# Kernel tuning notes

Hardware: AMD Instinct MI355X
Metric: run time of the kernel (lower is better)

The kernel has to match this reference:

```python
import jax, jax.numpy as jnp
import numpy as np

B, S, D, H, DFF = 2, 2048, 1024, 16, 4096
DK = D // H
EPS = 1e-6

def setup_inputs() -> dict:
    key = jax.random.key(0)
    ks = jax.random.split(key, 12)
    sc = 0.02
    inp = {
        "x": jax.random.normal(ks[0], (B, S, D), jnp.float32),
        "src_mask": jax.random.randint(ks[1], (B, 1, 1, S), 0, 2, jnp.int32),
        "wq": jax.random.normal(ks[2], (D, D), jnp.float32) * sc,
        "bq": jnp.zeros((D,), jnp.float32),
        "wk": jax.random.normal(ks[3], (D, D), jnp.float32) * sc,
        "bk": jnp.zeros((D,), jnp.float32),
        "wv": jax.random.normal(ks[4], (D, D), jnp.float32) * sc,
        "bv": jnp.zeros((D,), jnp.float32),
        "wo": jax.random.normal(ks[5], (D, D), jnp.float32) * sc,
        "bo": jnp.zeros((D,), jnp.float32),
        "w1": jax.random.normal(ks[6], (DFF, D), jnp.float32) * sc,
        "b1": jnp.zeros((DFF,), jnp.float32),
        "w2": jax.random.normal(ks[7], (D, DFF), jnp.float32) * sc,
        "b2": jnp.zeros((D,), jnp.float32),
        "a1": jnp.ones((1,), jnp.float32),
        "be1": jnp.zeros((1,), jnp.float32),
        "a2": jnp.ones((1,), jnp.float32),
        "be2": jnp.zeros((1,), jnp.float32),
    }
    return inp

def layer_norm(x, alpha, beta):
    # custom LN: unbiased std (ddof=1), scalar alpha/beta, divide by (std + eps)
    mean = jnp.mean(x, axis=-1, keepdims=True)
    std = jnp.std(x, axis=-1, keepdims=True, ddof=1)
    return alpha * (x - mean) / (std + EPS) + beta

def mha(x, mask, wq, bq, wk, bk, wv, bv, wo, bo):
    q = (x @ wq.T + bq).reshape(B, S, H, DK).transpose(0, 2, 1, 3)  # [B,H,S,DK]
    k = (x @ wk.T + bk).reshape(B, S, H, DK).transpose(0, 2, 1, 3)
    v = (x @ wv.T + bv).reshape(B, S, H, DK).transpose(0, 2, 1, 3)
    scores = jnp.einsum('bhqd,bhkd->bhqk', q, k) / jnp.sqrt(jnp.float32(DK))
    scores = jnp.where(mask == 0, jnp.float32(-1e9), scores)
    attn = jax.nn.softmax(scores, axis=-1)
    out = jnp.einsum('bhqk,bhkd->bhqd', attn, v)
    out = out.transpose(0, 2, 1, 3).reshape(B, S, D)
    return out @ wo.T + bo

def ffn(x, w1, b1, w2, b2):
    h = jax.nn.relu(x @ w1.T + b1)
    return h @ w2.T + b2

def reference(x, src_mask, wq, bq, wk, bk, wv, bv, wo, bo, w1, b1, w2, b2, a1, be1, a2, be2):
    # pre-norm residual 1: self-attention
    x = x + mha(layer_norm(x, a1, be1), src_mask, wq, bq, wk, bk, wv, bv, wo, bo)
    # pre-norm residual 2: FFN
    x = x + ffn(layer_norm(x, a2, be2), w1, b1, w2, b2)
    return x
```

## Files before the change

kernel.cpp:

```cpp
#include <hip/hip_runtime.h>

#define B_    2
#define S_    2048
#define D_    1024
#define H_    16
#define DK_   64
#define DFF_  4096
#define MROWS (B_*S_)

typedef float f32x4 __attribute__((ext_vector_type(4)));
typedef __bf16 bf16x8 __attribute__((ext_vector_type(8)));

static __device__ __forceinline__ unsigned short f2bf(float f) {
    union { float f; unsigned u; } a; a.f = f;
    unsigned u = a.u;
    u += 0x7FFF + ((u >> 16) & 1);
    return (unsigned short)(u >> 16);
}

static __device__ __forceinline__ void gload16(const unsigned short* g, unsigned short* l) {
    __builtin_amdgcn_global_load_lds((const __attribute__((address_space(1))) void*)g,
                                     (__attribute__((address_space(3))) void*)l, 16, 0, 0);
}

__global__ void cast_kernel(const float* __restrict__ in, unsigned short* __restrict__ out) {
    int i = blockIdx.x * blockDim.x + threadIdx.x;
    float4 v = ((const float4*)in)[i];
    ushort4 o;
    o.x = f2bf(v.x); o.y = f2bf(v.y); o.z = f2bf(v.z); o.w = f2bf(v.w);
    ((ushort4*)out)[i] = o;
}

__global__ __launch_bounds__(256) void ln_kernel(const float* __restrict__ x,
                                                 const float* __restrict__ alphap,
                                                 const float* __restrict__ betap,
                                                 unsigned short* __restrict__ out) {
    int row = blockIdx.x;
    int t = threadIdx.x;
    const float* xr = x + (size_t)row * D_;
    float4 v = ((const float4*)xr)[t];
    float s  = v.x + v.y + v.z + v.w;
    float s2 = v.x*v.x + v.y*v.y + v.z*v.z + v.w*v.w;
    #pragma unroll
    for (int o = 1; o < 64; o <<= 1) { s += __shfl_xor(s, o); s2 += __shfl_xor(s2, o); }
    __shared__ float ss[4], ss2[4];
    if ((t & 63) == 0) { ss[t >> 6] = s; ss2[t >> 6] = s2; }
    __syncthreads();
    float S  = ss[0] + ss[1] + ss[2] + ss[3];
    float S2 = ss2[0] + ss2[1] + ss2[2] + ss2[3];
    float mean = S * (1.f / (float)D_);
    float var  = (S2 - S * mean) / (float)(D_ - 1);
    float alpha = alphap[0], beta = betap[0];
    float inv = alpha / (sqrtf(fmaxf(var, 0.f)) + 1e-6f);
    ushort4 o4;
    o4.x = f2bf((v.x - mean) * inv + beta);
    o4.y = f2bf((v.y - mean) * inv + beta);
    o4.z = f2bf((v.z - mean) * inv + beta);
    o4.w = f2bf((v.w - mean) * inv + beta);
    ((ushort4*)(out + (size_t)row * D_))[t] = o4;
}

template<int BN, int EPI, int BIAS_ROW>
__global__ __launch_bounds__(256) void gemm_bt(const unsigned short* __restrict__ A,
                                               const unsigned short* __restrict__ W,
                                               const float* __restrict__ bias,
                                               const float* __restrict__ resid,
                                               unsigned short* __restrict__ outb,
                                               float* __restrict__ outf,
                                               int M, int N, int K) {
    constexpr int NI = BN / 32;
    __shared__ __align__(16) unsigned short As[128 * 64];
    __shared__ __align__(16) unsigned short Bs[BN * 64];
    const int t = threadIdx.x, lane = t & 63, w = t >> 6;
    const int m0 = blockIdx.y * 128, n0 = blockIdx.x * BN;
    const int wm = (w & 1) * 64;
    const int wn = (BN == 128) ? (w >> 1) * 64 : (w >> 1) * 32;
    const int l15 = lane & 15, l4 = lane >> 4;
    const int ar0 = w * 8 + (lane >> 3);
    const int ac0 = (lane & 7) * 8;

    f32x4 acc[4][NI];
    f32x4 z4 = {0.f, 0.f, 0.f, 0.f};
    #pragma unroll
    for (int i = 0; i < 4; i++)
        #pragma unroll
        for (int j = 0; j < NI; j++) acc[i][j] = z4;

    const unsigned short* Ap = A + (size_t)m0 * K;
    const unsigned short* Wp = W + (size_t)n0 * K;

    for (int k0 = 0; k0 < K; k0 += 64) {
        #pragma unroll
        for (int j = 0; j < 4; j++)
            gload16(Ap + (size_t)(j*32 + ar0) * K + k0 + ac0, &As[(j*4 + w) * 512]);
        #pragma unroll
        for (int j = 0; j < BN/32; j++)
            gload16(Wp + (size_t)(j*32 + ar0) * K + k0 + ac0, &Bs[(j*4 + w) * 512]);
        __syncthreads();

        #pragma unroll
        for (int ks = 0; ks < 2; ks++) {
            bf16x8 af[4], bfr[NI];
            #pragma unroll
            for (int mi = 0; mi < 4; mi++)
                af[mi] = *(const bf16x8*)&As[(wm + mi*16 + l15)*64 + ks*32 + l4*8];
            #pragma unroll
            for (int ni = 0; ni < NI; ni++)
                bfr[ni] = *(const bf16x8*)&Bs[(wn + ni*16 + l15)*64 + ks*32 + l4*8];
            #pragma unroll
            for (int mi = 0; mi < 4; mi++)
                #pragma unroll
                for (int ni = 0; ni < NI; ni++)
                    acc[mi][ni] = __builtin_amdgcn_mfma_f32_16x16x32_bf16(af[mi], bfr[ni], acc[mi][ni], 0, 0, 0);
        }
        __syncthreads();
    }

    #pragma unroll
    for (int mi = 0; mi < 4; mi++) {
        #pragma unroll
        for (int ni = 0; ni < NI; ni++) {
            int gc = n0 + wn + ni*16 + l15;
            float bc = BIAS_ROW ? 0.f : bias[gc];
            #pragma unroll
            for (int j = 0; j < 4; j++) {
                int gr = m0 + wm + mi*16 + 4*l4 + j;
                float val = acc[mi][ni][j] + (BIAS_ROW ? bias[gr] : bc);
                if (EPI == 1) val = fmaxf(val, 0.f);
                if (EPI == 2) {
                    val += resid[(size_t)gr * N + gc];
                    outf[(size_t)gr * N + gc] = val;
                } else {
                    outb[(size_t)gr * N + gc] = f2bf(val);
                }
            }
        }
    }
}

__global__ __launch_bounds__(256) void attn_kernel(const unsigned short* __restrict__ q,
                                                   const unsigned short* __restrict__ k,
                                                   const unsigned short* __restrict__ vt,
                                                   const int* __restrict__ mask,
                                                   unsigned short* __restrict__ out) {
    __shared__ __align__(16) unsigned short Ks[64][72], Vs[64][72], Ps[64][72];
    __shared__ int mS[64];
    const int t = threadIdx.x, lane = t & 63, w = t >> 6;
    const int l15 = lane & 15, l4 = lane >> 4;
    const int bh = blockIdx.y, b = bh >> 4, h = bh & 15;
    const int q0 = blockIdx.x * 64;
    const size_t headoff = ((size_t)b * S_) * D_ + (size_t)h * DK_;
    const unsigned short* qb = q + headoff + (size_t)q0 * D_;
    const unsigned short* kb = k + headoff;
    const unsigned short* vtb = vt + (size_t)(h * DK_) * MROWS + (size_t)b * S_;

    bf16x8 aq[2];
    #pragma unroll
    for (int ks = 0; ks < 2; ks++)
        aq[ks] = *(const bf16x8*)(qb + (size_t)(w*16 + l15) * D_ + ks*32 + l4*8);

    float m_[4], l_[4];
    f32x4 accd[4];
    f32x4 z4 = {0.f, 0.f, 0.f, 0.f};
    #pragma unroll
    for (int j = 0; j < 4; j++) { m_[j] = -INFINITY; l_[j] = 0.f; }
    #pragma unroll
    for (int dt = 0; dt < 4; dt++) accd[dt] = z4;

    const int r_ = t >> 3, c8_ = (t & 7) * 8;

    for (int kv0 = 0; kv0 < S_; kv0 += 64) {
        #pragma unroll
        for (int p = 0; p < 2; p++) {
            int r = r_ + p * 32;
            *(uint4*)&Ks[r][c8_] = *(const uint4*)(kb  + (size_t)(kv0 + r) * D_ + c8_);
            *(uint4*)&Vs[r][c8_] = *(const uint4*)(vtb + (size_t)r * MROWS + kv0 + c8_);
        }
        if (t < 64) mS[t] = mask[(size_t)b * S_ + kv0 + t];
        __syncthreads();

        f32x4 sc[4];
        #pragma unroll
        for (int nt = 0; nt < 4; nt++) sc[nt] = z4;
        #pragma unroll
        for (int nt = 0; nt < 4; nt++)
            #pragma unroll
            for (int ks = 0; ks < 2; ks++) {
                bf16x8 bk8 = *(const bf16x8*)&Ks[nt*16 + l15][ks*32 + 8*l4];
                sc[nt] = __builtin_amdgcn_mfma_f32_16x16x32_bf16(aq[ks], bk8, sc[nt], 0, 0, 0);
            }

        float sv[4][4];
        int mk[4];
        #pragma unroll
        for (int nt = 0; nt < 4; nt++) mk[nt] = mS[nt*16 + l15];
        #pragma unroll
        for (int nt = 0; nt < 4; nt++)
            #pragma unroll
            for (int j = 0; j < 4; j++)
                sv[nt][j] = (mk[nt] == 0) ? -1e9f : sc[nt][j] * 0.125f;

        float esc[4], rs[4];
        #pragma unroll
        for (int j = 0; j < 4; j++) {
            float mxx = fmaxf(fmaxf(sv[0][j], sv[1][j]), fmaxf(sv[2][j], sv[3][j]));
            #pragma unroll
            for (int o = 1; o < 16; o <<= 1) mxx = fmaxf(mxx, __shfl_xor(mxx, o));
            float mn = fmaxf(m_[j], mxx);
            esc[j] = __expf(m_[j] - mn);
            m_[j] = mn;
            rs[j] = 0.f;
        }
        float p[4][4];
        #pragma unroll
        for (int nt = 0; nt < 4; nt++)
            #pragma unroll
            for (int j = 0; j < 4; j++) { p[nt][j] = __expf(sv[nt][j] - m_[j]); rs[j] += p[nt][j]; }
        #pragma unroll
        for (int j = 0; j < 4; j++) {
            #pragma unroll
            for (int o = 1; o < 16; o <<= 1) rs[j] += __shfl_xor(rs[j], o);
            l_[j] = l_[j] * esc[j] + rs[j];
        }
        #pragma unroll
        for (int dt = 0; dt < 4; dt++)
            #pragma unroll
            for (int j = 0; j < 4; j++) accd[dt][j] *= esc[j];

        #pragma unroll
        for (int nt = 0; nt < 4; nt++)
            #pragma unroll
            for (int j = 0; j < 4; j++)
                Ps[w*16 + 4*l4 + j][nt*16 + l15] = f2bf(p[nt][j]);

        bf16x8 pa[2];
        #pragma unroll
        for (int ks = 0; ks < 2; ks++) pa[ks] = *(const bf16x8*)&Ps[w*16 + l15][ks*32 + 8*l4];
        #pragma unroll
        for (int dt = 0; dt < 4; dt++)
            #pragma unroll
            for (int ks = 0; ks < 2; ks++) {
                bf16x8 vv8 = *(const bf16x8*)&Vs[dt*16 + l15][ks*32 + 8*l4];
                accd[dt] = __builtin_amdgcn_mfma_f32_16x16x32_bf16(pa[ks], vv8, accd[dt], 0, 0, 0);
            }
        __syncthreads();
    }

    unsigned short* ob = out + headoff + (size_t)q0 * D_;
    #pragma unroll
    for (int j = 0; j < 4; j++) {
        float inv = 1.f / l_[j];
        int r = w*16 + 4*l4 + j;
        #pragma unroll
        for (int dt = 0; dt < 4; dt++)
            ob[(size_t)r * D_ + dt*16 + l15] = f2bf(accd[dt][j] * inv);
    }
}

extern "C" void kernel_launch(void* const* d_in, const int* in_sizes, int n_in,
                              void* d_out, int out_size, void* d_ws, size_t ws_size,
                              hipStream_t stream) {
    const float* x    = (const float*)d_in[0];
    const int*   mask = (const int*)d_in[1];
    const float* wq = (const float*)d_in[2];
    const float* bq = (const float*)d_in[3];
    const float* wk = (const float*)d_in[4];
    const float* bk = (const float*)d_in[5];
    const float* wv = (const float*)d_in[6];
    const float* bv = (const float*)d_in[7];
    const float* wo = (const float*)d_in[8];
    const float* bo = (const float*)d_in[9];
    const float* w1 = (const float*)d_in[10];
    const float* b1 = (const float*)d_in[11];
    const float* w2 = (const float*)d_in[12];
    const float* b2 = (const float*)d_in[13];
    const float* a1  = (const float*)d_in[14];
    const float* be1 = (const float*)d_in[15];
    const float* a2  = (const float*)d_in[16];
    const float* be2 = (const float*)d_in[17];
    float* out = (float*)d_out;

    char* ws = (char*)d_ws;
    unsigned short* wqb = (unsigned short*)(ws + (0ull  << 20));
    unsigned short* wkb = (unsigned short*)(ws + (2ull  << 20));
    unsigned short* wvb = (unsigned short*)(ws + (4ull  << 20));
    unsigned short* wob = (unsigned short*)(ws + (6ull  << 20));
    unsigned short* w1b = (unsigned short*)(ws + (8ull  << 20));
    unsigned short* w2b = (unsigned short*)(ws + (16ull << 20));
    unsigned short* xn  = (unsigned short*)(ws + (24ull << 20));
    unsigned short* qq  = (unsigned short*)(ws + (32ull << 20));
    unsigned short* kk  = (unsigned short*)(ws + (40ull << 20));
    unsigned short* vtb = (unsigned short*)(ws + (48ull << 20));
    unsigned short* hh  = qq;
    float*          x1  = (float*)(ws + (64ull << 20));

    dim3 blk(256);

    cast_kernel<<<D_*D_/1024,   blk, 0, stream>>>(wq, wqb);
    cast_kernel<<<D_*D_/1024,   blk, 0, stream>>>(wk, wkb);
    cast_kernel<<<D_*D_/1024,   blk, 0, stream>>>(wv, wvb);
    cast_kernel<<<D_*D_/1024,   blk, 0, stream>>>(wo, wob);
    cast_kernel<<<DFF_*D_/1024, blk, 0, stream>>>(w1, w1b);
    cast_kernel<<<DFF_*D_/1024, blk, 0, stream>>>(w2, w2b);

    ln_kernel<<<MROWS, blk, 0, stream>>>(x, a1, be1, xn);

    dim3 gqk(D_/64, MROWS/128);
    gemm_bt<64,0,0><<<gqk, blk, 0, stream>>>(xn, wqb, bq, nullptr, qq, nullptr, MROWS, D_, D_);
    gemm_bt<64,0,0><<<gqk, blk, 0, stream>>>(xn, wkb, bk, nullptr, kk, nullptr, MROWS, D_, D_);
    dim3 gvt(MROWS/64, D_/128);
    gemm_bt<64,0,1><<<gvt, blk, 0, stream>>>(wvb, xn, bv, nullptr, vtb, nullptr, D_, MROWS, D_);

    dim3 ga(S_/64, B_*H_);
    attn_kernel<<<ga, blk, 0, stream>>>(qq, kk, vtb, mask, xn);

    gemm_bt<64,2,0><<<gqk, blk, 0, stream>>>(xn, wob, bo, x, nullptr, x1, MROWS, D_, D_);

    ln_kernel<<<MROWS, blk, 0, stream>>>(x1, a2, be2, xn);

    dim3 gf1(DFF_/128, MROWS/128);
    gemm_bt<128,1,0><<<gf1, blk, 0, stream>>>(xn, w1b, b1, nullptr, hh, nullptr, MROWS, DFF_, D_);

    gemm_bt<64,2,0><<<gqk, blk, 0, stream>>>(hh, w2b, b2, x1, nullptr, out, MROWS, D_, DFF_);
}
```

Baseline: 469.3 us.

## Fuse weight casts, merge Q/K projection, swizzle attention LDS, lazy softmax rescale

Replaces the six weight-cast launches with one prep kernel that also concatenates the Q and K biases. Q and K are now produced by a single 2048-wide GEMM with BN=128 that folds the 1/sqrt(dk) scale into the Q half. The attention kernel reads the interleaved QK buffer and uses XOR-swizzled unpadded LDS tiles for K, V and P instead of padded rows. It also skips the online-softmax rescale of the accumulators when no row maximum increases across the wavefront. Float-to-bf16 conversion now uses the compiler's native cast. Together these cut launch count, fuse two GEMMs and trim attention ALU and LDS bank-conflict cost, at the price of more complex indexing.

```diff
diff --git a/kernel.cpp b/kernel.cpp
--- a/kernel.cpp
+++ b/kernel.cpp
@@ -12,10 +12,9 @@
 typedef __bf16 bf16x8 __attribute__((ext_vector_type(8)));
 
 static __device__ __forceinline__ unsigned short f2bf(float f) {
-    union { float f; unsigned u; } a; a.f = f;
-    unsigned u = a.u;
-    u += 0x7FFF + ((u >> 16) & 1);
-    return (unsigned short)(u >> 16);
+    union { __bf16 h; unsigned short u; } cv;
+    cv.h = (__bf16)f;
+    return cv.u;
 }
 
 static __device__ __forceinline__ void gload16(const unsigned short* g, unsigned short* l) {
@@ -23,12 +22,36 @@
                                      (__attribute__((address_space(3))) void*)l, 16, 0, 0);
 }
 
-__global__ void cast_kernel(const float* __restrict__ in, unsigned short* __restrict__ out) {
-    int i = blockIdx.x * blockDim.x + threadIdx.x;
-    float4 v = ((const float4*)in)[i];
+__global__ __launch_bounds__(256) void prep_kernel(
+    const float* __restrict__ wq, const float* __restrict__ wk,
+    const float* __restrict__ wv, const float* __restrict__ wo,
+    const float* __restrict__ w1, const float* __restrict__ w2,
+    const float* __restrict__ bq, const float* __restrict__ bk,
+    unsigned short* __restrict__ wqkb, unsigned short* __restrict__ wvb,
+    unsigned short* __restrict__ wob, unsigned short* __restrict__ w1b,
+    unsigned short* __restrict__ w2b, float* __restrict__ bqk) {
+    int blk = blockIdx.x;
+    if (blk >= 12288) {
+        int t0 = threadIdx.x * 8;
+        #pragma unroll
+        for (int i = 0; i < 8; i++) {
+            int j = t0 + i;
+            bqk[j] = (j < 1024) ? bq[j] : bk[j - 1024];
+        }
+        return;
+    }
+    const float* src; unsigned short* dst; int lb;
+    if      (blk < 1024) { src = wq; dst = wqkb;             lb = blk;        }
+    else if (blk < 2048) { src = wk; dst = wqkb + (1 << 20); lb = blk - 1024; }
+    else if (blk < 3072) { src = wv; dst = wvb;              lb = blk - 2048; }
+    else if (blk < 4096) { src = wo; dst = wob;              lb = blk - 3072; }
+    else if (blk < 8192) { src = w1; dst = w1b;              lb = blk - 4096; }
+    else                 { src = w2; dst = w2b;              lb = blk - 8192; }
+    int i4 = lb * 256 + threadIdx.x;
+    float4 v = ((const float4*)src)[i4];
     ushort4 o;
     o.x = f2bf(v.x); o.y = f2bf(v.y); o.z = f2bf(v.z); o.w = f2bf(v.w);
-    ((ushort4*)out)[i] = o;
+    ((ushort4*)dst)[i4] = o;
 }
 
 __global__ __launch_bounds__(256) void ln_kernel(const float* __restrict__ x,
@@ -60,7 +83,7 @@
     ((ushort4*)(out + (size_t)row * D_))[t] = o4;
 }
 
-template<int BN, int EPI, int BIAS_ROW>
+template<int BN, int EPI, int BIAS_ROW, int QSCALE>
 __global__ __launch_bounds__(256) void gemm_bt(const unsigned short* __restrict__ A,
                                                const unsigned short* __restrict__ W,
                                                const float* __restrict__ bias,
@@ -127,6 +150,7 @@
                 int gr = m0 + wm + mi*16 + 4*l4 + j;
                 float val = acc[mi][ni][j] + (BIAS_ROW ? bias[gr] : bc);
                 if (EPI == 1) val = fmaxf(val, 0.f);
+                if (QSCALE) { if (gc < (N >> 1)) val *= 0.125f; }
                 if (EPI == 2) {
                     val += resid[(size_t)gr * N + gc];
                     outf[(size_t)gr * N + gc] = val;
@@ -138,26 +162,24 @@
     }
 }
 
-__global__ __launch_bounds__(256) void attn_kernel(const unsigned short* __restrict__ q,
-                                                   const unsigned short* __restrict__ k,
+__global__ __launch_bounds__(256) void attn_kernel(const unsigned short* __restrict__ qk,
                                                    const unsigned short* __restrict__ vt,
                                                    const int* __restrict__ mask,
                                                    unsigned short* __restrict__ out) {
-    __shared__ __align__(16) unsigned short Ks[64][72], Vs[64][72], Ps[64][72];
+    __shared__ __align__(16) unsigned short Ks[64*64], Vs[64*64], Ps[64*64];
     __shared__ int mS[64];
     const int t = threadIdx.x, lane = t & 63, w = t >> 6;
     const int l15 = lane & 15, l4 = lane >> 4;
     const int bh = blockIdx.y, b = bh >> 4, h = bh & 15;
     const int q0 = blockIdx.x * 64;
-    const size_t headoff = ((size_t)b * S_) * D_ + (size_t)h * DK_;
-    const unsigned short* qb = q + headoff + (size_t)q0 * D_;
-    const unsigned short* kb = k + headoff;
+    const unsigned short* qb  = qk + ((size_t)(b * S_ + q0)) * 2048 + h * DK_;
+    const unsigned short* kb  = qk + ((size_t)(b * S_)) * 2048 + 1024 + h * DK_;
     const unsigned short* vtb = vt + (size_t)(h * DK_) * MROWS + (size_t)b * S_;
 
     bf16x8 aq[2];
     #pragma unroll
     for (int ks = 0; ks < 2; ks++)
-        aq[ks] = *(const bf16x8*)(qb + (size_t)(w*16 + l15) * D_ + ks*32 + l4*8);
+        aq[ks] = *(const bf16x8*)(qb + (size_t)(w*16 + l15) * 2048 + ks*32 + l4*8);
 
     float m_[4], l_[4];
     f32x4 accd[4];
@@ -167,14 +189,16 @@
     #pragma unroll
     for (int dt = 0; dt < 4; dt++) accd[dt] = z4;
 
-    const int r_ = t >> 3, c8_ = (t & 7) * 8;
+    const int r_  = t >> 3, c8_ = (t & 7) * 8;
+    const int cs_ = c8_ ^ ((r_ & 7) << 3);
+    const int rsw = (l15 & 7) << 3;
 
     for (int kv0 = 0; kv0 < S_; kv0 += 64) {
         #pragma unroll
         for (int p = 0; p < 2; p++) {
             int r = r_ + p * 32;
-            *(uint4*)&Ks[r][c8_] = *(const uint4*)(kb  + (size_t)(kv0 + r) * D_ + c8_);
-            *(uint4*)&Vs[r][c8_] = *(const uint4*)(vtb + (size_t)r * MROWS + kv0 + c8_);
+            *(uint4*)&Ks[r*64 + cs_] = *(const uint4*)(kb  + (size_t)(kv0 + r) * 2048 + c8_);
+            *(uint4*)&Vs[r*64 + cs_] = *(const uint4*)(vtb + (size_t)r * MROWS + kv0 + c8_);
         }
         if (t < 64) mS[t] = mask[(size_t)b * S_ + kv0 + t];
         __syncthreads();
@@ -186,7 +210,7 @@
         for (int nt = 0; nt < 4; nt++)
             #pragma unroll
             for (int ks = 0; ks < 2; ks++) {
-                bf16x8 bk8 = *(const bf16x8*)&Ks[nt*16 + l15][ks*32 + 8*l4];
+                bf16x8 bk8 = *(const bf16x8*)&Ks[(nt*16 + l15)*64 + ((ks*32 + 8*l4) ^ rsw)];
                 sc[nt] = __builtin_amdgcn_mfma_f32_16x16x32_bf16(aq[ks], bk8, sc[nt], 0, 0, 0);
             }
 
@@ -198,19 +222,29 @@
         for (int nt = 0; nt < 4; nt++)
             #pragma unroll
             for (int j = 0; j < 4; j++)
-                sv[nt][j] = (mk[nt] == 0) ? -1e9f : sc[nt][j] * 0.125f;
-
-        float esc[4], rs[4];
+                sv[nt][j] = (mk[nt] == 0) ? -1e9f : sc[nt][j];
+
+        float mx[4];
         #pragma unroll
         for (int j = 0; j < 4; j++) {
             float mxx = fmaxf(fmaxf(sv[0][j], sv[1][j]), fmaxf(sv[2][j], sv[3][j]));
             #pragma unroll
             for (int o = 1; o < 16; o <<= 1) mxx = fmaxf(mxx, __shfl_xor(mxx, o));
-            float mn = fmaxf(m_[j], mxx);
-            esc[j] = __expf(m_[j] - mn);
-            m_[j] = mn;
-            rs[j] = 0.f;
-        }
+            mx[j] = mxx;
+        }
+        bool upd = (mx[0] > m_[0]) | (mx[1] > m_[1]) | (mx[2] > m_[2]) | (mx[3] > m_[3]);
+        if (__any(upd)) {
+            #pragma unroll
+            for (int j = 0; j < 4; j++) {
+                float mn  = fmaxf(m_[j], mx[j]);
+                float esc = __expf(m_[j] - mn);
+                m_[j] = mn;
+                l_[j] *= esc;
+                #pragma unroll
+                for (int dt = 0; dt < 4; dt++) accd[dt][j] *= esc;
+            }
+        }
+        float rs[4] = {0.f, 0.f, 0.f, 0.f};
         float p[4][4];
         #pragma unroll
         for (int nt = 0; nt < 4; nt++)
@@ -220,33 +254,32 @@
         for (int j = 0; j < 4; j++) {
             #pragma unroll
             for (int o = 1; o < 16; o <<= 1) rs[j] += __shfl_xor(rs[j], o);
-            l_[j] = l_[j] * esc[j] + rs[j];
-        }
+            l_[j] += rs[j];
+        }
+
+        #pragma unroll
+        for (int nt = 0; nt < 4; nt++)
+            #pragma unroll
+            for (int j = 0; j < 4; j++) {
+                int pr = w*16 + 4*l4 + j;
+                Ps[pr*64 + ((nt*16 + l15) ^ (((4*l4 + j) & 7) << 3))] = f2bf(p[nt][j]);
+            }
+
+        bf16x8 pa[2];
+        #pragma unroll
+        for (int ks = 0; ks < 2; ks++)
+            pa[ks] = *(const bf16x8*)&Ps[(w*16 + l15)*64 + ((ks*32 + 8*l4) ^ rsw)];
         #pragma unroll
         for (int dt = 0; dt < 4; dt++)
             #pragma unroll
-            for (int j = 0; j < 4; j++) accd[dt][j] *= esc[j];
-
-        #pragma unroll
-        for (int nt = 0; nt < 4; nt++)
-            #pragma unroll
-            for (int j = 0; j < 4; j++)
-                Ps[w*16 + 4*l4 + j][nt*16 + l15] = f2bf(p[nt][j]);
-
-        bf16x8 pa[2];
-        #pragma unroll
-        for (int ks = 0; ks < 2; ks++) pa[ks] = *(const bf16x8*)&Ps[w*16 + l15][ks*32 + 8*l4];
-        #pragma unroll
-        for (int dt = 0; dt < 4; dt++)
-            #pragma unroll
             for (int ks = 0; ks < 2; ks++) {
-                bf16x8 vv8 = *(const bf16x8*)&Vs[dt*16 + l15][ks*32 + 8*l4];
+                bf16x8 vv8 = *(const bf16x8*)&Vs[(dt*16 + l15)*64 + ((ks*32 + 8*l4) ^ rsw)];
                 accd[dt] = __builtin_amdgcn_mfma_f32_16x16x32_bf16(pa[ks], vv8, accd[dt], 0, 0, 0);
             }
         __syncthreads();
     }
 
-    unsigned short* ob = out + headoff + (size_t)q0 * D_;
+    unsigned short* ob = out + ((size_t)(b * S_ + q0)) * D_ + h * DK_;
     #pragma unroll
     for (int j = 0; j < 4; j++) {
         float inv = 1.f / l_[j];
@@ -281,45 +314,41 @@
     float* out = (float*)d_out;
 
     char* ws = (char*)d_ws;
-    unsigned short* wqb = (unsigned short*)(ws + (0ull  << 20));
-    unsigned short* wkb = (unsigned short*)(ws + (2ull  << 20));
-    unsigned short* wvb = (unsigned short*)(ws + (4ull  << 20));
-    unsigned short* wob = (unsigned short*)(ws + (6ull  << 20));
-    unsigned short* w1b = (unsigned short*)(ws + (8ull  << 20));
-    unsigned short* w2b = (unsigned short*)(ws + (16ull << 20));
-    unsigned short* xn  = (unsigned short*)(ws + (24ull << 20));
-    unsigned short* qq  = (unsigned short*)(ws + (32ull << 20));
-    unsigned short* kk  = (unsigned short*)(ws + (40ull << 20));
-    unsigned short* vtb = (unsigned short*)(ws + (48ull << 20));
-    unsigned short* hh  = qq;
-    float*          x1  = (float*)(ws + (64ull << 20));
+    unsigned short* wqkb = (unsigned short*)(ws + (0ull  << 20));
+    unsigned short* wvb  = (unsigned short*)(ws + (4ull  << 20));
+    unsigned short* wob  = (unsigned short*)(ws + (6ull  << 20));
+    unsigned short* w1b  = (unsigned short*)(ws + (8ull  << 20));
+    unsigned short* w2b  = (unsigned short*)(ws + (16ull << 20));
+    unsigned short* xn   = (unsigned short*)(ws + (24ull << 20));
+    unsigned short* qkb  = (unsigned short*)(ws + (32ull << 20));
+    unsigned short* vtb  = (unsigned short*)(ws + (48ull << 20));
+    float*          bqk  = (float*)         (ws + (60ull << 20));
+    unsigned short* hh   = qkb;
+    float*          x1   = (float*)(ws + (64ull << 20));
 
     dim3 blk(256);
 
-    cast_kernel<<<D_*D_/1024,   blk, 0, stream>>>(wq, wqb);
-    cast_kernel<<<D_*D_/1024,   blk, 0, stream>>>(wk, wkb);
-    cast_kernel<<<D_*D_/1024,   blk, 0, stream>>>(wv, wvb);
-    cast_kernel<<<D_*D_/1024,   blk, 0, stream>>>(wo, wob);
-    cast_kernel<<<DFF_*D_/1024, blk, 0, stream>>>(w1, w1b);
-    cast_kernel<<<DFF_*D_/1024, blk, 0, stream>>>(w2, w2b);
+    prep_kernel<<<12289, blk, 0, stream>>>(wq, wk, wv, wo, w1, w2, bq, bk,
+                                           wqkb, wvb, wob, w1b, w2b, bqk);
 
     ln_kernel<<<MROWS, blk, 0, stream>>>(x, a1, be1, xn);
 
-    dim3 gqk(D_/64, MROWS/128);
-    gemm_bt<64,0,0><<<gqk, blk, 0, stream>>>(xn, wqb, bq, nullptr, qq, nullptr, MROWS, D_, D_);
-    gemm_bt<64,0,0><<<gqk, blk, 0, stream>>>(xn, wkb, bk, nullptr, kk, nullptr, MROWS, D_, D_);
+    dim3 gqk(2048/128, MROWS/128);
+    gemm_bt<128,0,0,1><<<gqk, blk, 0, stream>>>(xn, wqkb, bqk, nullptr, qkb, nullptr, MROWS, 2048, D_);
+
     dim3 gvt(MROWS/64, D_/128);
-    gemm_bt<64,0,1><<<gvt, blk, 0, stream>>>(wvb, xn, bv, nullptr, vtb, nullptr, D_, MROWS, D_);
+    gemm_bt<64,0,1,0><<<gvt, blk, 0, stream>>>(wvb, xn, bv, nullptr, vtb, nullptr, D_, MROWS, D_);
 
     dim3 ga(S_/64, B_*H_);
-    attn_kernel<<<ga, blk, 0, stream>>>(qq, kk, vtb, mask, xn);
-
-    gemm_bt<64,2,0><<<gqk, blk, 0, stream>>>(xn, wob, bo, x, nullptr, x1, MROWS, D_, D_);
+    attn_kernel<<<ga, blk, 0, stream>>>(qkb, vtb, mask, xn);
+
+    dim3 go(D_/64, MROWS/128);
+    gemm_bt<64,2,0,0><<<go, blk, 0, stream>>>(xn, wob, bo, x, nullptr, x1, MROWS, D_, D_);
 
     ln_kernel<<<MROWS, blk, 0, stream>>>(x1, a2, be2, xn);
 
     dim3 gf1(DFF_/128, MROWS/128);
-    gemm_bt<128,1,0><<<gf1, blk, 0, stream>>>(xn, w1b, b1, nullptr, hh, nullptr, MROWS, DFF_, D_);
-
-    gemm_bt<64,2,0><<<gqk, blk, 0, stream>>>(hh, w2b, b2, x1, nullptr, out, MROWS, D_, DFF_);
-}
+    gemm_bt<128,1,0,0><<<gf1, blk, 0, stream>>>(xn, w1b, b1, nullptr, hh, nullptr, MROWS, DFF_, D_);
+
+    gemm_bt<64,2,0,0><<<go, blk, 0, stream>>>(hh, w2b, b2, x1, nullptr, out, MROWS, D_, DFF_);
+}
```

After: 447.3 us. 4.7% less time.
